# Performance work log

Hardware: AMD Instinct MI355X
Metric: run time of the kernel (lower is better)

## Reference

```python
import jax, jax.numpy as jnp
import numpy as np

ACTION_SCALE = 0.01
LOG_STD_MIN, LOG_STD_MAX = -20.0, 2.0


def setup_inputs() -> dict:
    key = jax.random.key(0)
    k1, k2, k3 = jax.random.split(key, 3)
    B, N, D = 8, 1024, 128
    kv = jax.random.normal(k1, (B, N, 4 * D), dtype=jnp.float32)
    positions = jax.random.normal(k2, (B, N, 3), dtype=jnp.float32)
    eps = jax.random.normal(k3, (B, N, 3), dtype=jnp.float32)  # standard-normal sample for rsample
    return {"kv": kv, "positions": positions, "eps": eps}


def reference(kv, positions, eps):
    # Split Atomwise output into mean/std key-value embeddings: each [B, N, D]
    k_mu, v_mu, k_sigma, v_sigma = jnp.split(kv, 4, axis=-1)

    # Low-rank attention-like pairwise scores: [B, N, N]
    rel_shifts_mean = jnp.einsum("bid,bjd->bij", k_mu, v_mu)
    rel_shifts_log_std = jnp.einsum("bid,bjd->bij", k_sigma, v_sigma)

    # All-pairs unit displacement vectors: [B, N, N, 3]
    P = positions[:, :, None, :] - positions[:, None, :, :]
    norm = jnp.linalg.norm(P, axis=-1) + 1e-8
    P = P / norm[..., None]

    # Weighted sum over the j axis (torch dim=-2): [B, N, 3]
    actions_mean = jnp.einsum("bijc,bij->bic", P, rel_shifts_mean)
    actions_log_std = jnp.clip(
        jnp.einsum("bijc,bij->bic", P, rel_shifts_log_std), LOG_STD_MIN, LOG_STD_MAX
    )
    actions_std = jnp.exp(actions_log_std)

    # TanhNormal rsample (training branch) with externally supplied noise eps
    pre_tanh = actions_mean + actions_std * eps
    actions = jnp.tanh(pre_tanh)

    # Normal log-prob minus tanh log-det-Jacobian
    normal_lp = (
        -0.5 * ((pre_tanh - actions_mean) / actions_std) ** 2
        - actions_log_std
        - 0.5 * jnp.log(2.0 * jnp.pi)
    )
    log_det = (
        2.0 * jnp.log(2.0)
        + jax.nn.log_sigmoid(2.0 * pre_tanh)
        + jax.nn.log_sigmoid(-2.0 * pre_tanh)
    )
    log_prob = jnp.sum(normal_lp - log_det, axis=(1, 2))[:, None]  # [B, 1]

    actions = actions * ACTION_SCALE
    # change-of-variables correction for the action_scale factor
    n_dims = pre_tanh.shape[1] * pre_tanh.shape[2]
    log_prob = log_prob - n_dims * jnp.log(ACTION_SCALE)
    return actions, log_prob
```

## Files before the change

kernel.cpp:

```cpp
#include <hip/hip_runtime.h>
#include <math.h>


#define NTOK 1024
#define LPCONST 14147.0828114f

typedef __bf16 bf16x8 __attribute__((ext_vector_type(8)));
typedef float f32x4 __attribute__((ext_vector_type(4)));
#define MFMA(a, b, c) __builtin_amdgcn_mfma_f32_16x16x32_bf16(a, b, c, 0, 0, 0)

__device__ __forceinline__ unsigned short to_bf16(float x) {
    return (unsigned short)((__float_as_uint(x) + 0x8000u) >> 16);
}

template <int CTRL>
__device__ __forceinline__ float dpp_add(float v) {
    int y = __builtin_amdgcn_update_dpp(0, __float_as_int(v), CTRL, 0xf, 0xf, true);
    return v + __int_as_float(y);
}
__device__ __forceinline__ float red16(float v) {
    v = dpp_add<0xB1>(v);
    v = dpp_add<0x4E>(v);
    v = dpp_add<0x141>(v);
    v = dpp_add<0x140>(v);
    return v;
}

__device__ __forceinline__ float softplusf(float z) {
    return z > 20.f ? z : log1pf(expf(z));
}

__global__ __launch_bounds__(256) void prepass_kernel(
    const float* __restrict__ kv, unsigned short* __restrict__ frag,
    float* __restrict__ out)
{
    const int t = blockIdx.x * 256 + threadIdx.x;
    if (t < 8) out[8 * NTOK * 3 + t] = LPCONST;

    const int lane = t & 63;
    const int kc   = (t >> 6) & 3;
    const int tile = (t >> 8) & 63;
    const int b    = (t >> 14) & 7;
    const int side = t >> 17;

    const int row = tile * 16 + (lane & 15);
    const int kof = kc * 32 + (lane >> 4) * 8;
    const float* gp = kv + ((size_t)b * NTOK + row) * 512 + side * 128 + kof;
    const float4 m0 = *(const float4*)gp;
    const float4 m1 = *(const float4*)(gp + 4);
    const float4 s0 = *(const float4*)(gp + 256);
    const float4 s1 = *(const float4*)(gp + 260);

    unsigned short* cp = frag + (size_t)side * 2097152 +
                         (size_t)(b * 64 + tile) * 4096 + kc * 1024 + lane * 8;
    ushort4 h0, h1;
    h0.x = to_bf16(m0.x); h0.y = to_bf16(m0.y); h0.z = to_bf16(m0.z); h0.w = to_bf16(m0.w);
    h1.x = to_bf16(m1.x); h1.y = to_bf16(m1.y); h1.z = to_bf16(m1.z); h1.w = to_bf16(m1.w);
    *(ushort4*)(cp + 0) = h0; *(ushort4*)(cp + 4) = h1;
    h0.x = to_bf16(s0.x); h0.y = to_bf16(s0.y); h0.z = to_bf16(s0.z); h0.w = to_bf16(s0.w);
    h1.x = to_bf16(s1.x); h1.y = to_bf16(s1.y); h1.z = to_bf16(s1.z); h1.w = to_bf16(s1.w);
    *(ushort4*)(cp + 512) = h0; *(ushort4*)(cp + 516) = h1;
}

__global__ __launch_bounds__(512) void actor_kernel(
    const unsigned short* __restrict__ frag, const float* __restrict__ pos,
    float* __restrict__ partial)
{
    const int t = threadIdx.x;
    const int w = t >> 6;
    const int lane = t & 63;
    const int q = lane >> 4;
    const int r16 = lane & 15;
    const int b    = blockIdx.x & 7;
    const int jh   = (blockIdx.x >> 3) & 1;
    const int ithx = blockIdx.x >> 4;
    const int i0 = ithx * 32;

    const unsigned short* fragK = frag;
    const unsigned short* fragV = frag + 2097152;
    const float* posb = pos + (size_t)b * NTOK * 3;

    __shared__ float spos[NTOK * 3];
    __shared__ float wacc[8 * 32 * 6];

    for (int u = t; u < 768; u += 512)
        *(float4*)&spos[u * 4] = *(const float4*)&posb[u * 4];

    const unsigned short* kp =
        fragK + (size_t)(b * 64 + ithx * 2) * 4096 + lane * 8;
    bf16x8 Km0[4], Ks0[4], Km1[4], Ks1[4];
    #pragma unroll
    for (int kc = 0; kc < 4; ++kc) {
        Km0[kc] = *(const bf16x8*)(kp + kc * 1024);
        Ks0[kc] = *(const bf16x8*)(kp + kc * 1024 + 512);
        Km1[kc] = *(const bf16x8*)(kp + 4096 + kc * 1024);
        Ks1[kc] = *(const bf16x8*)(kp + 4096 + kc * 1024 + 512);
    }

    __syncthreads();

    const float pix0 = spos[(i0 + r16) * 3 + 0];
    const float piy0 = spos[(i0 + r16) * 3 + 1];
    const float piz0 = spos[(i0 + r16) * 3 + 2];
    const float pix1 = spos[(i0 + 16 + r16) * 3 + 0];
    const float piy1 = spos[(i0 + 16 + r16) * 3 + 1];
    const float piz1 = spos[(i0 + 16 + r16) * 3 + 2];

    float am[2][3] = {};
    float al[2][3] = {};

    const int jtile0 = jh * 32 + w * 4;
    const unsigned short* vbase =
        fragV + (size_t)(b * 64 + jtile0) * 4096 + lane * 8;

    #pragma unroll
    for (int jt = 0; jt < 4; ++jt) {
        const unsigned short* vp = vbase + jt * 4096;
        f32x4 accm0 = (f32x4){0.f, 0.f, 0.f, 0.f};
        f32x4 accs0 = (f32x4){0.f, 0.f, 0.f, 0.f};
        f32x4 accm1 = (f32x4){0.f, 0.f, 0.f, 0.f};
        f32x4 accs1 = (f32x4){0.f, 0.f, 0.f, 0.f};
        #pragma unroll
        for (int kc = 0; kc < 4; ++kc) {
            const bf16x8 Vm = *(const bf16x8*)(vp + kc * 1024);
            const bf16x8 Vs = *(const bf16x8*)(vp + kc * 1024 + 512);
            accm0 = MFMA(Vm, Km0[kc], accm0);
            accs0 = MFMA(Vs, Ks0[kc], accs0);
            accm1 = MFMA(Vm, Km1[kc], accm1);
            accs1 = MFMA(Vs, Ks1[kc], accs1);
        }
        const int jbase = (jtile0 + jt) * 16 + q * 4;
        #pragma unroll
        for (int reg = 0; reg < 4; ++reg) {
            const float* pj = &spos[(jbase + reg) * 3];
            {
                const float dx = pix0 - pj[0];
                const float dy = piy0 - pj[1];
                const float dz = piz0 - pj[2];
                const float d2 = dx * dx + dy * dy + dz * dz;
                const float inv = d2 > 0.f ? rsqrtf(d2) : 0.f;
                const float wm = accm0[reg] * inv;
                const float ws = accs0[reg] * inv;
                am[0][0] = fmaf(dx, wm, am[0][0]);
                am[0][1] = fmaf(dy, wm, am[0][1]);
                am[0][2] = fmaf(dz, wm, am[0][2]);
                al[0][0] = fmaf(dx, ws, al[0][0]);
                al[0][1] = fmaf(dy, ws, al[0][1]);
                al[0][2] = fmaf(dz, ws, al[0][2]);
            }
            {
                const float dx = pix1 - pj[0];
                const float dy = piy1 - pj[1];
                const float dz = piz1 - pj[2];
                const float d2 = dx * dx + dy * dy + dz * dz;
                const float inv = d2 > 0.f ? rsqrtf(d2) : 0.f;
                const float wm = accm1[reg] * inv;
                const float ws = accs1[reg] * inv;
                am[1][0] = fmaf(dx, wm, am[1][0]);
                am[1][1] = fmaf(dy, wm, am[1][1]);
                am[1][2] = fmaf(dz, wm, am[1][2]);
                al[1][0] = fmaf(dx, ws, al[1][0]);
                al[1][1] = fmaf(dy, ws, al[1][1]);
                al[1][2] = fmaf(dz, ws, al[1][2]);
            }
        }
    }

    #pragma unroll
    for (int tile = 0; tile < 2; ++tile)
        #pragma unroll
        for (int c = 0; c < 3; ++c) {
            float vm = am[tile][c], vl = al[tile][c];
            vm += __shfl_xor(vm, 16, 64); vm += __shfl_xor(vm, 32, 64);
            vl += __shfl_xor(vl, 16, 64); vl += __shfl_xor(vl, 32, 64);
            am[tile][c] = vm; al[tile][c] = vl;
        }

    if (lane < 16) {
        #pragma unroll
        for (int tile = 0; tile < 2; ++tile) {
            float* p = wacc + (w * 32 + tile * 16 + r16) * 6;
            p[0] = am[tile][0]; p[1] = am[tile][1]; p[2] = am[tile][2];
            p[3] = al[tile][0]; p[4] = al[tile][1]; p[5] = al[tile][2];
        }
    }
    __syncthreads();
    if (t < 192) {
        float v = 0.f;
        #pragma unroll
        for (int ww = 0; ww < 8; ++ww) v += wacc[ww * 192 + t];
        const int row = t / 6, c = t - row * 6;
        partial[((size_t)((jh * 8 + b) * NTOK) + i0 + row) * 6 + c] = v;
    }
}

__global__ __launch_bounds__(64) void actor_tail_kernel(
    const float* __restrict__ partial, const float* __restrict__ eps,
    float* __restrict__ out)
{
    const int b = blockIdx.x >> 4;
    const int i = (blockIdx.x & 15) * 64 + threadIdx.x;
    const int gi = b * NTOK + i;

    float am[3], al[3];
    {
        const float* p0 = partial + (((size_t)0 * 8 + b) * NTOK + i) * 6;
        const float* p1 = partial + (((size_t)1 * 8 + b) * NTOK + i) * 6;
        am[0] = p0[0] + p1[0]; am[1] = p0[1] + p1[1]; am[2] = p0[2] + p1[2];
        al[0] = p0[3] + p1[3]; al[1] = p0[4] + p1[4]; al[2] = p0[5] + p1[5];
    }

    float lp = 0.f;
    #pragma unroll
    for (int c = 0; c < 3; ++c) {
        const float als = fminf(fmaxf(al[c], -20.f), 2.f);
        const float sd = expf(als);
        const float e = eps[gi * 3 + c];
        const float pre = fmaf(sd, e, am[c]);
        out[gi * 3 + c] = tanhf(pre) * 0.01f;
        const float t2 = 2.f * pre;
        lp += -0.5f * e * e - als - 2.3052328944f + softplusf(t2) + softplusf(-t2);
    }

    #pragma unroll
    for (int m = 1; m < 64; m <<= 1) lp += __shfl_xor(lp, m, 64);
    if (threadIdx.x == 0) atomicAdd(out + NTOK * 8 * 3 + b, lp);
}

extern "C" void kernel_launch(void* const* d_in, const int* in_sizes, int n_in,
                              void* d_out, int out_size, void* d_ws, size_t ws_size,
                              hipStream_t stream) {
    const float* kv = (const float*)d_in[0];
    const float* pos = (const float*)d_in[1];
    const float* eps = (const float*)d_in[2];
    float* out = (float*)d_out;
    unsigned short* frag = (unsigned short*)d_ws;
    float* partial = (float*)((char*)d_ws + 8388608);

    prepass_kernel<<<dim3(1024), 256, 0, stream>>>(kv, frag, out);
    actor_kernel<<<dim3(512), 512, 0, stream>>>(frag, pos, partial);
    actor_tail_kernel<<<dim3(128), 64, 0, stream>>>(partial, eps, out);
}
```

Measured before the change: 89.17 us.

## Stage K fragments in LDS and widen i-tile to 64 rows with 4-way j split

```diff
diff --git a/kernel.cpp b/kernel.cpp
--- a/kernel.cpp
+++ b/kernel.cpp
@@ -11,19 +11,6 @@
 
 __device__ __forceinline__ unsigned short to_bf16(float x) {
     return (unsigned short)((__float_as_uint(x) + 0x8000u) >> 16);
-}
-
-template <int CTRL>
-__device__ __forceinline__ float dpp_add(float v) {
-    int y = __builtin_amdgcn_update_dpp(0, __float_as_int(v), CTRL, 0xf, 0xf, true);
-    return v + __int_as_float(y);
-}
-__device__ __forceinline__ float red16(float v) {
-    v = dpp_add<0xB1>(v);
-    v = dpp_add<0x4E>(v);
-    v = dpp_add<0x141>(v);
-    v = dpp_add<0x140>(v);
-    return v;
 }
 
 __device__ __forceinline__ float softplusf(float z) {
@@ -71,103 +58,97 @@
     const int lane = t & 63;
     const int q = lane >> 4;
     const int r16 = lane & 15;
-    const int b    = blockIdx.x & 7;
-    const int jh   = (blockIdx.x >> 3) & 1;
-    const int ithx = blockIdx.x >> 4;
-    const int i0 = ithx * 32;
+    const int b   = blockIdx.x & 7;
+    const int jh  = (blockIdx.x >> 3) & 3;
+    const int ibx = blockIdx.x >> 5;
+    const int i0 = ibx * 64;
 
     const unsigned short* fragK = frag;
     const unsigned short* fragV = frag + 2097152;
     const float* posb = pos + (size_t)b * NTOK * 3;
 
+    __shared__ unsigned short sK[16384];
     __shared__ float spos[NTOK * 3];
-    __shared__ float wacc[8 * 32 * 6];
-
+    __shared__ float wacc[8 * 64 * 6];
+
+    {
+        const unsigned short* kg =
+            fragK + (size_t)(b * 64 + ibx * 4) * 4096 + t * 32;
+        #pragma unroll
+        for (int r = 0; r < 4; ++r)
+            *(ushort4*)&sK[t * 32 + r * 4] = *(const ushort4*)(kg + r * 4);
+        const unsigned short* kg2 = kg + 16;
+        #pragma unroll
+        for (int r = 0; r < 4; ++r)
+            *(ushort4*)&sK[t * 32 + 16 + r * 4] = *(const ushort4*)(kg2 + r * 4);
+    }
     for (int u = t; u < 768; u += 512)
         *(float4*)&spos[u * 4] = *(const float4*)&posb[u * 4];
-
-    const unsigned short* kp =
-        fragK + (size_t)(b * 64 + ithx * 2) * 4096 + lane * 8;
-    bf16x8 Km0[4], Ks0[4], Km1[4], Ks1[4];
-    #pragma unroll
-    for (int kc = 0; kc < 4; ++kc) {
-        Km0[kc] = *(const bf16x8*)(kp + kc * 1024);
-        Ks0[kc] = *(const bf16x8*)(kp + kc * 1024 + 512);
-        Km1[kc] = *(const bf16x8*)(kp + 4096 + kc * 1024);
-        Ks1[kc] = *(const bf16x8*)(kp + 4096 + kc * 1024 + 512);
-    }
-
     __syncthreads();
 
-    const float pix0 = spos[(i0 + r16) * 3 + 0];
-    const float piy0 = spos[(i0 + r16) * 3 + 1];
-    const float piz0 = spos[(i0 + r16) * 3 + 2];
-    const float pix1 = spos[(i0 + 16 + r16) * 3 + 0];
-    const float piy1 = spos[(i0 + 16 + r16) * 3 + 1];
-    const float piz1 = spos[(i0 + 16 + r16) * 3 + 2];
-
-    float am[2][3] = {};
-    float al[2][3] = {};
-
-    const int jtile0 = jh * 32 + w * 4;
+    float pix[4], piy[4], piz[4];
+    #pragma unroll
+    for (int tile = 0; tile < 4; ++tile) {
+        pix[tile] = spos[(i0 + tile * 16 + r16) * 3 + 0];
+        piy[tile] = spos[(i0 + tile * 16 + r16) * 3 + 1];
+        piz[tile] = spos[(i0 + tile * 16 + r16) * 3 + 2];
+    }
+
+    float am[4][3] = {};
+    float al[4][3] = {};
+
+    const int jtile0 = jh * 16 + w * 2;
     const unsigned short* vbase =
         fragV + (size_t)(b * 64 + jtile0) * 4096 + lane * 8;
-
-    #pragma unroll
-    for (int jt = 0; jt < 4; ++jt) {
+    const int klofs = lane * 8;
+
+    #pragma unroll
+    for (int jt = 0; jt < 2; ++jt) {
         const unsigned short* vp = vbase + jt * 4096;
-        f32x4 accm0 = (f32x4){0.f, 0.f, 0.f, 0.f};
-        f32x4 accs0 = (f32x4){0.f, 0.f, 0.f, 0.f};
-        f32x4 accm1 = (f32x4){0.f, 0.f, 0.f, 0.f};
-        f32x4 accs1 = (f32x4){0.f, 0.f, 0.f, 0.f};
+        f32x4 accm[4], accs[4];
+        #pragma unroll
+        for (int tile = 0; tile < 4; ++tile) {
+            accm[tile] = (f32x4){0.f, 0.f, 0.f, 0.f};
+            accs[tile] = (f32x4){0.f, 0.f, 0.f, 0.f};
+        }
         #pragma unroll
         for (int kc = 0; kc < 4; ++kc) {
             const bf16x8 Vm = *(const bf16x8*)(vp + kc * 1024);
             const bf16x8 Vs = *(const bf16x8*)(vp + kc * 1024 + 512);
-            accm0 = MFMA(Vm, Km0[kc], accm0);
-            accs0 = MFMA(Vs, Ks0[kc], accs0);
-            accm1 = MFMA(Vm, Km1[kc], accm1);
-            accs1 = MFMA(Vs, Ks1[kc], accs1);
+            #pragma unroll
+            for (int tile = 0; tile < 4; ++tile) {
+                const bf16x8 Km = *(const bf16x8*)&sK[tile * 4096 + kc * 1024 + klofs];
+                const bf16x8 Ks = *(const bf16x8*)&sK[tile * 4096 + kc * 1024 + 512 + klofs];
+                accm[tile] = MFMA(Vm, Km, accm[tile]);
+                accs[tile] = MFMA(Vs, Ks, accs[tile]);
+            }
         }
         const int jbase = (jtile0 + jt) * 16 + q * 4;
         #pragma unroll
         for (int reg = 0; reg < 4; ++reg) {
             const float* pj = &spos[(jbase + reg) * 3];
-            {
-                const float dx = pix0 - pj[0];
-                const float dy = piy0 - pj[1];
-                const float dz = piz0 - pj[2];
+            const float pjx = pj[0], pjy = pj[1], pjz = pj[2];
+            #pragma unroll
+            for (int tile = 0; tile < 4; ++tile) {
+                const float dx = pix[tile] - pjx;
+                const float dy = piy[tile] - pjy;
+                const float dz = piz[tile] - pjz;
                 const float d2 = dx * dx + dy * dy + dz * dz;
                 const float inv = d2 > 0.f ? rsqrtf(d2) : 0.f;
-                const float wm = accm0[reg] * inv;
-                const float ws = accs0[reg] * inv;
-                am[0][0] = fmaf(dx, wm, am[0][0]);
-                am[0][1] = fmaf(dy, wm, am[0][1]);
-                am[0][2] = fmaf(dz, wm, am[0][2]);
-                al[0][0] = fmaf(dx, ws, al[0][0]);
-                al[0][1] = fmaf(dy, ws, al[0][1]);
-                al[0][2] = fmaf(dz, ws, al[0][2]);
+                const float wm = accm[tile][reg] * inv;
+                const float ws = accs[tile][reg] * inv;
+                am[tile][0] = fmaf(dx, wm, am[tile][0]);
+                am[tile][1] = fmaf(dy, wm, am[tile][1]);
+                am[tile][2] = fmaf(dz, wm, am[tile][2]);
+                al[tile][0] = fmaf(dx, ws, al[tile][0]);
+                al[tile][1] = fmaf(dy, ws, al[tile][1]);
+                al[tile][2] = fmaf(dz, ws, al[tile][2]);
             }
-            {
-                const float dx = pix1 - pj[0];
-                const float dy = piy1 - pj[1];
-                const float dz = piz1 - pj[2];
-                const float d2 = dx * dx + dy * dy + dz * dz;
-                const float inv = d2 > 0.f ? rsqrtf(d2) : 0.f;
-                const float wm = accm1[reg] * inv;
-                const float ws = accs1[reg] * inv;
-                am[1][0] = fmaf(dx, wm, am[1][0]);
-                am[1][1] = fmaf(dy, wm, am[1][1]);
-                am[1][2] = fmaf(dz, wm, am[1][2]);
-                al[1][0] = fmaf(dx, ws, al[1][0]);
-                al[1][1] = fmaf(dy, ws, al[1][1]);
-                al[1][2] = fmaf(dz, ws, al[1][2]);
-            }
-        }
-    }
-
-    #pragma unroll
-    for (int tile = 0; tile < 2; ++tile)
+        }
+    }
+
+    #pragma unroll
+    for (int tile = 0; tile < 4; ++tile)
         #pragma unroll
         for (int c = 0; c < 3; ++c) {
             float vm = am[tile][c], vl = al[tile][c];
@@ -178,17 +159,17 @@
 
     if (lane < 16) {
         #pragma unroll
-        for (int tile = 0; tile < 2; ++tile) {
-            float* p = wacc + (w * 32 + tile * 16 + r16) * 6;
+        for (int tile = 0; tile < 4; ++tile) {
+            float* p = wacc + (w * 64 + tile * 16 + r16) * 6;
             p[0] = am[tile][0]; p[1] = am[tile][1]; p[2] = am[tile][2];
             p[3] = al[tile][0]; p[4] = al[tile][1]; p[5] = al[tile][2];
         }
     }
     __syncthreads();
-    if (t < 192) {
+    if (t < 384) {
         float v = 0.f;
         #pragma unroll
-        for (int ww = 0; ww < 8; ++ww) v += wacc[ww * 192 + t];
+        for (int ww = 0; ww < 8; ++ww) v += wacc[ww * 384 + t];
         const int row = t / 6, c = t - row * 6;
         partial[((size_t)((jh * 8 + b) * NTOK) + i0 + row) * 6 + c] = v;
     }
@@ -202,12 +183,15 @@
     const int i = (blockIdx.x & 15) * 64 + threadIdx.x;
     const int gi = b * NTOK + i;
 
-    float am[3], al[3];
-    {
-        const float* p0 = partial + (((size_t)0 * 8 + b) * NTOK + i) * 6;
-        const float* p1 = partial + (((size_t)1 * 8 + b) * NTOK + i) * 6;
-        am[0] = p0[0] + p1[0]; am[1] = p0[1] + p1[1]; am[2] = p0[2] + p1[2];
-        al[0] = p0[3] + p1[3]; al[1] = p0[4] + p1[4]; al[2] = p0[5] + p1[5];
+    float am[3] = {}, al[3] = {};
+    #pragma unroll
+    for (int jh = 0; jh < 4; ++jh) {
+        const float* p = partial + (((size_t)jh * 8 + b) * NTOK + i) * 6;
+        const float2 v0 = *(const float2*)(p);
+        const float2 v1 = *(const float2*)(p + 2);
+        const float2 v2 = *(const float2*)(p + 4);
+        am[0] += v0.x; am[1] += v0.y; am[2] += v1.x;
+        al[0] += v1.y; al[1] += v2.x; al[2] += v2.y;
     }
 
     float lp = 0.f;
```

Measured after the change: 88.05 us. Within noise of the previous version (-1.3%).
